# Performance work log

Measured on AMD Instinct MI355X. Metric: run time of the kernel, lower is better.

The kernel has to match this reference:

```python
import jax, jax.numpy as jnp
import numpy as np

L, B, D = 4096, 4, 1024

def setup_inputs() -> dict:
    key = jax.random.key(0)
    k1, k2, k3, k4 = jax.random.split(key, 4)
    return {
        "x": jax.random.normal(k1, (L, B, D), dtype=jnp.float32),
        "lmlg": jax.random.normal(k2, (D,), dtype=jnp.float32),
        "theta": jax.random.normal(k3, (D,), dtype=jnp.float32),
        "last_conv_init": jax.random.normal(k4, (D,), dtype=jnp.float32),
    }

def reference(x, lmlg, theta, last_conv_init):
    seq_len, batch, dim = x.shape
    # per-channel decay*rotation: c = gamma * e^{i*theta}, gamma = exp(-exp(lmlg))
    gamma = jnp.exp(-jnp.exp(lmlg))                       # [D]
    c = gamma * jnp.exp(1j * theta)                       # [D] complex64
    # causal filter c^n for n = 0..L-1
    n = jnp.arange(seq_len)[:, None]                      # [L,1]
    filt = c[None, :] ** n                                # [L,D] complex64
    # linear (causal) convolution via zero-padded FFT of length 2L
    filt_fft = jnp.fft.fft(filt, n=2 * seq_len, axis=0)   # [2L,D]
    x_fft = jnp.fft.fft(x, n=2 * seq_len, axis=0)         # [2L,B,D]
    conv_filter_x = jnp.fft.ifft(filt_fft[:, None, :] * x_fft, axis=0)[:seq_len]  # [L,B,D]
    # carry-in state (fresh state = last_conv_init expanded; detached in torch)
    last_conv = jax.lax.stop_gradient(
        jnp.broadcast_to(last_conv_init.astype(conv_filter_x.dtype), (batch, dim))
    )                                                     # [B,D]
    conv_with_past = conv_filter_x + last_conv[None, :, :] * filt[:, None, :] * c[None, None, :]
    return conv_with_past.real * x
```

## Files before the change

kernel.cpp:

```cpp
#include <hip/hip_runtime.h>


#define L_  4096
#define B_  4
#define D_  1024
#define BD_ (B_ * D_)

__global__ __launch_bounds__(256) void sc_sum(
    const float* __restrict__ x,
    const float* __restrict__ lmlg,
    const float* __restrict__ theta,
    float2* __restrict__ ws, int ch) {
  const int t   = threadIdx.x;
  const int bid = blockIdx.x;
  const int db  = bid & 3;
  const int b   = (bid >> 2) & (B_ - 1);
  const int k   = bid >> 4;
  const int d   = (db << 8) + t;

  const float lg = lmlg[d], th = theta[d];
  const float g  = expf(-expf(lg));
  const float cr = g * cosf(th), ci = g * sinf(th);

  float sr = 0.f, si = 0.f;
  const float* xp = x + (size_t)k * ch * BD_ + (size_t)b * D_ + d;
#pragma unroll 8
  for (int j = 0; j < ch; ++j) {
    float xv = xp[(size_t)j * BD_];
    float nr = fmaf(cr, sr, fmaf(-ci, si, xv));
    float ni = fmaf(cr, si, ci * sr);
    sr = nr; si = ni;
  }
  ws[(size_t)(k * B_ + b) * D_ + d] = make_float2(sr, si);
}

__global__ __launch_bounds__(256) void sc_out(
    const float* __restrict__ x,
    const float* __restrict__ lmlg,
    const float* __restrict__ theta,
    const float* __restrict__ init,
    const float2* __restrict__ ws,
    float* __restrict__ out, int ch) {
  const int t   = threadIdx.x;
  const int bid = blockIdx.x;
  const int db  = bid & 3;
  const int b   = (bid >> 2) & (B_ - 1);
  const int k   = bid >> 4;
  const int d   = (db << 8) + t;

  const float lg = lmlg[d], th = theta[d];
  const float e  = expf(lg);
  const float g  = expf(-e);
  const float cr = g * cosf(th), ci = g * sinf(th);

  const float chf = (float)ch;
  const float G   = expf(-e * chf);
  const float Cr  = G * cosf(th * chf), Ci = G * sinf(th * chf);

  float hr = init[d], hi = 0.f;
  const float2* sp = ws + (size_t)b * D_ + d;
#pragma unroll 4
  for (int kk = 0; kk < k; ++kk) {
    float2 s = sp[(size_t)kk * BD_];
    float nr = fmaf(Cr, hr, fmaf(-Ci, hi, s.x));
    float ni = fmaf(Cr, hi, fmaf(Ci, hr, s.y));
    hr = nr; hi = ni;
  }

  const size_t off = (size_t)k * ch * BD_ + (size_t)b * D_ + d;
  const float* xp = x + off;
  float*       op = out + off;
#pragma unroll 8
  for (int j = 0; j < ch; ++j) {
    float xv = xp[(size_t)j * BD_];
    float nr = fmaf(cr, hr, fmaf(-ci, hi, xv));
    float ni = fmaf(cr, hi, ci * hr);
    hr = nr; hi = ni;
    op[(size_t)j * BD_] = nr * xv;
  }
}

__global__ __launch_bounds__(256) void sc_full(
    const float* __restrict__ x, const float* __restrict__ lmlg,
    const float* __restrict__ theta, const float* __restrict__ init,
    float* __restrict__ out) {
  const int idx = blockIdx.x * 256 + threadIdx.x;
  const int d   = idx & (D_ - 1);
  float g = expf(-expf(lmlg[d]));
  float cr = g * cosf(theta[d]), ci = g * sinf(theta[d]);
  float hr = init[d], hi = 0.f;
  const float* xp = x + idx;
  float*       op = out + idx;
  for (int n = 0; n < L_; ++n) {
    float xv = xp[(size_t)n * BD_];
    float nr = fmaf(cr, hr, fmaf(-ci, hi, xv));
    float ni = fmaf(cr, hi, ci * hr);
    hr = nr; hi = ni;
    op[(size_t)n * BD_] = nr * xv;
  }
}

extern "C" void kernel_launch(void* const* d_in, const int* in_sizes, int n_in,
                              void* d_out, int out_size, void* d_ws, size_t ws_size,
                              hipStream_t stream) {
  const float* x     = (const float*)d_in[0];
  const float* lmlg  = (const float*)d_in[1];
  const float* theta = (const float*)d_in[2];
  const float* init  = (const float*)d_in[3];
  float*  out = (float*)d_out;
  float2* ws  = (float2*)d_ws;

  const size_t row_bytes = (size_t)BD_ * sizeof(float2);
  int nc = 128;
  while (nc > 1 && (size_t)nc * row_bytes > ws_size) nc >>= 1;

  if (nc >= 2 && (size_t)nc * row_bytes <= ws_size) {
    const int ch = L_ / nc;
    const int grid = nc * B_ * (D_ / 256);
    sc_sum<<<grid, 256, 0, stream>>>(x, lmlg, theta, ws, ch);
    sc_out<<<grid, 256, 0, stream>>>(x, lmlg, theta, init, ws, out, ch);
  } else {
    sc_full<<<BD_ / 256, 256, 0, stream>>>(x, lmlg, theta, init, out);
  }
}
```

Measured before the change: 135.2 us.

## Fuse chunked scan into single-pass decoupled look-back kernel with register-cached inputs

```diff
diff --git a/kernel.cpp b/kernel.cpp
--- a/kernel.cpp
+++ b/kernel.cpp
@@ -1,82 +1,137 @@
 #include <hip/hip_runtime.h>
 
 
-#define L_  4096
-#define B_  4
-#define D_  1024
-#define BD_ (B_ * D_)
+#define L_   4096
+#define B_   4
+#define D_   1024
+#define BD_  (B_ * D_)
+#define NC_  128
+#define CH_  (L_ / NC_)
+#define NBLK_ (NC_ * B_ * 4)
+#define SUMN_ ((size_t)NC_ * B_ * D_)
 
-__global__ __launch_bounds__(256) void sc_sum(
-    const float* __restrict__ x,
-    const float* __restrict__ lmlg,
-    const float* __restrict__ theta,
-    float2* __restrict__ ws, int ch) {
-  const int t   = threadIdx.x;
-  const int bid = blockIdx.x;
-  const int db  = bid & 3;
-  const int b   = (bid >> 2) & (B_ - 1);
-  const int k   = bid >> 4;
-  const int d   = (db << 8) + t;
+#define WS_FLAGS_OFF  64
+#define WS_SUM_OFF    16384
+#define WS_BYTES_NEEDED (WS_SUM_OFF + 2u * SUMN_ * sizeof(float2))
 
-  const float lg = lmlg[d], th = theta[d];
-  const float g  = expf(-expf(lg));
-  const float cr = g * cosf(th), ci = g * sinf(th);
-
-  float sr = 0.f, si = 0.f;
-  const float* xp = x + (size_t)k * ch * BD_ + (size_t)b * D_ + d;
-#pragma unroll 8
-  for (int j = 0; j < ch; ++j) {
-    float xv = xp[(size_t)j * BD_];
-    float nr = fmaf(cr, sr, fmaf(-ci, si, xv));
-    float ni = fmaf(cr, si, ci * sr);
-    sr = nr; si = ni;
-  }
-  ws[(size_t)(k * B_ + b) * D_ + d] = make_float2(sr, si);
+__global__ __launch_bounds__(256) void sc_init(unsigned int* wsu) {
+  for (int i = threadIdx.x; i < 4096; i += 256) wsu[i] = 0u;
 }
 
-__global__ __launch_bounds__(256) void sc_out(
+__global__ __launch_bounds__(256) void sc_fused(
     const float* __restrict__ x,
     const float* __restrict__ lmlg,
     const float* __restrict__ theta,
     const float* __restrict__ init,
-    const float2* __restrict__ ws,
-    float* __restrict__ out, int ch) {
+    unsigned int* __restrict__ wsu,
+    float* __restrict__ out) {
+  __shared__ int s_blk;
+  __shared__ int s_m;
+
+  unsigned int* ticket = wsu;
+  unsigned int* flags  = wsu + WS_FLAGS_OFF;
+  float2* part = (float2*)((char*)wsu + WS_SUM_OFF);
+  float2* incl = part + SUMN_;
+
+  if (threadIdx.x == 0)
+    s_blk = (int)__hip_atomic_fetch_add(ticket, 1u, __ATOMIC_RELAXED,
+                                        __HIP_MEMORY_SCOPE_AGENT);
+  __syncthreads();
+  const int blk = s_blk;
+  const int db  = blk & 3;
+  const int b   = (blk >> 2) & 3;
+  const int k   = blk >> 4;
   const int t   = threadIdx.x;
-  const int bid = blockIdx.x;
-  const int db  = bid & 3;
-  const int b   = (bid >> 2) & (B_ - 1);
-  const int k   = bid >> 4;
   const int d   = (db << 8) + t;
 
   const float lg = lmlg[d], th = theta[d];
   const float e  = expf(lg);
   const float g  = expf(-e);
   const float cr = g * cosf(th), ci = g * sinf(th);
+  const float chf = (float)CH_;
+  const float G  = expf(-e * chf);
+  const float Cr = G * cosf(th * chf), Ci = G * sinf(th * chf);
 
-  const float chf = (float)ch;
-  const float G   = expf(-e * chf);
-  const float Cr  = G * cosf(th * chf), Ci = G * sinf(th * chf);
-
-  float hr = init[d], hi = 0.f;
-  const float2* sp = ws + (size_t)b * D_ + d;
-#pragma unroll 4
-  for (int kk = 0; kk < k; ++kk) {
-    float2 s = sp[(size_t)kk * BD_];
-    float nr = fmaf(Cr, hr, fmaf(-Ci, hi, s.x));
-    float ni = fmaf(Cr, hi, fmaf(Ci, hr, s.y));
-    hr = nr; hi = ni;
+  const size_t off = (size_t)k * CH_ * BD_ + (size_t)b * D_ + d;
+  const float* xp = x + off;
+  float xv[CH_];
+  float sr = 0.f, si = 0.f;
+#pragma unroll
+  for (int j = 0; j < CH_; ++j) {
+    xv[j] = xp[(size_t)j * BD_];
+    float nr = fmaf(cr, sr, fmaf(-ci, si, xv[j]));
+    float ni = fmaf(cr, si, ci * sr);
+    sr = nr; si = ni;
   }
 
-  const size_t off = (size_t)k * ch * BD_ + (size_t)b * D_ + d;
-  const float* xp = x + off;
-  float*       op = out + off;
-#pragma unroll 8
-  for (int j = 0; j < ch; ++j) {
-    float xv = xp[(size_t)j * BD_];
-    float nr = fmaf(cr, hr, fmaf(-ci, hi, xv));
+  const size_t sidx = (size_t)(k * B_ + b) * D_ + d;
+  part[sidx] = make_float2(sr, si);
+  __syncthreads();
+  if (t == 0) {
+    __threadfence();
+    __hip_atomic_store(&flags[blk], 1u, __ATOMIC_RELEASE,
+                       __HIP_MEMORY_SCOPE_AGENT);
+  }
+
+  if (t == 0) {
+    int m = -1;
+    for (int kk = k - 1; kk >= 0; --kk) {
+      const int fidx = (kk << 4) | (b << 2) | db;
+      unsigned int f;
+      while ((f = __hip_atomic_load(&flags[fidx], __ATOMIC_RELAXED,
+                                    __HIP_MEMORY_SCOPE_AGENT)) == 0u)
+        __builtin_amdgcn_s_sleep(8);
+      if (f >= 2u) { m = kk; break; }
+    }
+    s_m = m;
+    __threadfence();
+  }
+  __syncthreads();
+  const int m = s_m;
+
+  float hr, hi;
+  {
+    float ar = 0.f, ai = 0.f;
+    float pr = 1.f, pi = 0.f;
+    for (int kk = k - 1; kk > m; --kk) {
+      float2 s = part[(size_t)(kk * B_ + b) * D_ + d];
+      ar = fmaf(pr, s.x, fmaf(-pi, s.y, ar));
+      ai = fmaf(pr, s.y, fmaf( pi, s.x, ai));
+      float npr = fmaf(pr, Cr, -pi * Ci);
+      float npi = fmaf(pr, Ci,  pi * Cr);
+      pr = npr; pi = npi;
+    }
+    if (m >= 0) {
+      float2 I = incl[(size_t)(m * B_ + b) * D_ + d];
+      ar = fmaf(pr, I.x, fmaf(-pi, I.y, ar));
+      ai = fmaf(pr, I.y, fmaf( pi, I.x, ai));
+    } else {
+      float iv = init[d];
+      ar = fmaf(pr, iv, ar);
+      ai = fmaf(pi, iv, ai);
+    }
+    hr = ar; hi = ai;
+  }
+
+  {
+    float Ir = fmaf(Cr, hr, fmaf(-Ci, hi, sr));
+    float Ii = fmaf(Cr, hi, fmaf( Ci, hr, si));
+    incl[sidx] = make_float2(Ir, Ii);
+  }
+  __syncthreads();
+  if (t == 0) {
+    __threadfence();
+    __hip_atomic_store(&flags[blk], 2u, __ATOMIC_RELEASE,
+                       __HIP_MEMORY_SCOPE_AGENT);
+  }
+
+  float* op = out + off;
+#pragma unroll
+  for (int j = 0; j < CH_; ++j) {
+    float nr = fmaf(cr, hr, fmaf(-ci, hi, xv[j]));
     float ni = fmaf(cr, hi, ci * hr);
     hr = nr; hi = ni;
-    op[(size_t)j * BD_] = nr * xv;
+    op[(size_t)j * BD_] = nr * xv[j];
   }
 }
 
@@ -107,18 +162,12 @@
   const float* lmlg  = (const float*)d_in[1];
   const float* theta = (const float*)d_in[2];
   const float* init  = (const float*)d_in[3];
-  float*  out = (float*)d_out;
-  float2* ws  = (float2*)d_ws;
+  float* out = (float*)d_out;
 
-  const size_t row_bytes = (size_t)BD_ * sizeof(float2);
-  int nc = 128;
-  while (nc > 1 && (size_t)nc * row_bytes > ws_size) nc >>= 1;
-
-  if (nc >= 2 && (size_t)nc * row_bytes <= ws_size) {
-    const int ch = L_ / nc;
-    const int grid = nc * B_ * (D_ / 256);
-    sc_sum<<<grid, 256, 0, stream>>>(x, lmlg, theta, ws, ch);
-    sc_out<<<grid, 256, 0, stream>>>(x, lmlg, theta, init, ws, out, ch);
+  if (ws_size >= (size_t)WS_BYTES_NEEDED) {
+    unsigned int* wsu = (unsigned int*)d_ws;
+    sc_init <<<1, 256, 0, stream>>>(wsu);
+    sc_fused<<<NBLK_, 256, 0, stream>>>(x, lmlg, theta, init, wsu, out);
   } else {
     sc_full<<<BD_ / 256, 256, 0, stream>>>(x, lmlg, theta, init, out);
   }
```

After: 451.4 us. 234% more time.
